# Kernel optimization log

Measured on AMD Instinct MI355X. Metric: run time of the kernel, lower is better.

Reference implementation:

```python
import jax, jax.numpy as jnp
import numpy as np

PAD_TOKEN_ID = 0
PAGE_SIZE = 64
BOUNDARY_IDS = (13, 30)


def setup_inputs() -> dict:
    B, L, V = 64, 16384, 32000
    P = L // PAGE_SIZE
    key = jax.random.key(0)
    k1, k2, k3 = jax.random.split(key, 3)
    input_ids = jax.random.randint(k1, (B, L), 0, V, dtype=jnp.int32)
    attention_mask = jnp.ones((B, L), dtype=jnp.int32)
    # token -> page index, exactly pos // page_size as SegmentPager would build
    token2page = jnp.broadcast_to(jnp.arange(L, dtype=jnp.int32) // PAGE_SIZE, (B, L))
    keep_pages = jax.random.bernoulli(k2, 0.3, (B, P))  # bool [B, P]
    query_pos = jax.random.randint(k3, (B,), 0, L, dtype=jnp.int32)
    return {
        'input_ids': input_ids,
        'attention_mask': attention_mask,
        'token2page': token2page,
        'keep_pages': keep_pages,
        'query_pos': query_pos,
    }


def reference(input_ids, attention_mask, token2page, keep_pages, query_pos):
    B, L = input_ids.shape
    valid = attention_mask.astype(bool)                         # token_valid [B,L]
    pos = jnp.arange(L, dtype=jnp.int32)

    # --- page-level keep mask gathered per token ---
    t2p = jnp.clip(token2page, 0, None)
    page_keep = jnp.take_along_axis(keep_pages, t2p, axis=1)    # [B,L] bool
    mask = valid & page_keep                                    # keep_token

    # --- force-keep the query tail: mask[qp:] |= valid[qp:] ---
    qp = jnp.clip(query_pos.astype(jnp.int32), 0, L - 1)        # [B]
    tail = pos[None, :] >= qp[:, None]
    mask = mask | (tail & valid)

    # --- sentence rescue in context [0, qp): if any token of a sentence is kept,
    #     keep all valid tokens of that sentence. Sentences are delimited by
    #     boundary tokens (segment = exclusive cumsum of boundary indicators). ---
    boundary = jnp.zeros_like(valid)
    for tid in BOUNDARY_IDS:
        boundary = boundary | (input_ids == tid)
    boundary = boundary & valid
    bcnt = boundary.astype(jnp.int32)
    seg = jnp.cumsum(bcnt, axis=1) - bcnt                       # sentence id per token
    in_ctx = pos[None, :] < qp[:, None]
    seg_d = jnp.where(in_ctx, seg, L)                           # dummy segment L for non-ctx
    flat_seg = (jnp.arange(B, dtype=jnp.int32)[:, None] * (L + 1) + seg_d).reshape(-1)
    keep_any = jax.ops.segment_max(mask.astype(jnp.int32).reshape(-1), flat_seg,
                                   num_segments=B * (L + 1))
    tok_keep = (keep_any[flat_seg] > 0).reshape(B, L)
    mask = mask | (in_ctx & valid & tok_keep)

    # --- fallback: if nothing kept, keep last valid token (or position 0) ---
    any_kept = mask.any(axis=1)
    any_valid = valid.any(axis=1)
    last_valid = jnp.where(any_valid, L - 1 - jnp.argmax(valid[:, ::-1], axis=1), 0)
    fallback = pos[None, :] == last_valid[:, None]
    mask = jnp.where(any_kept[:, None], mask, fallback)

    # --- stream compaction + left-justified padding (padded to L for static shape) ---
    order = jnp.argsort(jnp.logical_not(mask), axis=1)          # stable: kept indices first, in order
    lk = mask.sum(axis=1).astype(jnp.int32)                     # kept length per row
    attn = pos[None, :] < lk[:, None]
    ids_sorted = jnp.take_along_axis(input_ids, order, axis=1)
    ids_comp = jnp.where(attn, ids_sorted, PAD_TOKEN_ID)
    attn_comp = attn.astype(jnp.int32)
    pos_comp = jnp.where(attn, pos[None, :], 0)
    return ids_comp, attn_comp, pos_comp
```

## Files before the change

kernel.cpp:

```cpp
#include <hip/hip_runtime.h>
#include <stdint.h>

#define BB 64
#define LL 16384
#define PP 256
#define NT 1024
#define TT 16

__device__ __forceinline__ int block_exscan(int v, int tid, int* s_wave, int* s_total) {
    __syncthreads();
    const int lane = tid & 63;
    const int wv = tid >> 6;
    int inc = v;
#pragma unroll
    for (int off = 1; off < 64; off <<= 1) {
        int n = __shfl_up(inc, off, 64);
        if (lane >= off) inc += n;
    }
    if (lane == 63) s_wave[wv] = inc;
    __syncthreads();
    if (wv == 0) {
        int wval = (lane < 16) ? s_wave[lane] : 0;
        int winc = wval;
#pragma unroll
        for (int off = 1; off < 16; off <<= 1) {
            int n = __shfl_up(winc, off, 64);
            if (lane >= off) winc += n;
        }
        if (lane < 16) s_wave[lane] = winc - wval;
        if (lane == 15) *s_total = winc;
    }
    __syncthreads();
    return inc - v + s_wave[wv];
}

__global__ void __launch_bounds__(NT) seg_kernel(
    const int* __restrict__ g_ids,
    const int* __restrict__ g_amask,
    const int* __restrict__ g_t2p,
    const int* __restrict__ g_kp,
    const int* __restrict__ g_qp,
    int* __restrict__ g_out)
{
    __shared__ unsigned int segbits[LL / 32];
    __shared__ unsigned char kp[PP];
    __shared__ int s_wave[16];
    __shared__ int s_total;

    const int b = blockIdx.x;
    const int tid = threadIdx.x;
    const int tbase = tid * TT;
    const int rowoff = b * LL;

    for (int i = tid; i < LL / 32; i += NT) segbits[i] = 0u;
    if (tid < PP) kp[tid] = (g_kp[b * PP + tid] != 0);

    int qp = g_qp[b];
    qp = qp < 0 ? 0 : (qp > LL - 1 ? LL - 1 : qp);
    __syncthreads();

    int myids[TT];
    unsigned validbits = 0u, bndbits = 0u, mask1bits = 0u;
    {
        const int4* idp = (const int4*)(g_ids   + rowoff + tbase);
        const int4* amp = (const int4*)(g_amask + rowoff + tbase);
        const int4* tpp = (const int4*)(g_t2p   + rowoff + tbase);
#pragma unroll
        for (int jv = 0; jv < TT / 4; ++jv) {
            int4 iv = idp[jv];
            int4 av = amp[jv];
            int4 pv = tpp[jv];
            int idsv[4] = {iv.x, iv.y, iv.z, iv.w};
            int amv[4]  = {av.x, av.y, av.z, av.w};
            int tpv[4]  = {pv.x, pv.y, pv.z, pv.w};
#pragma unroll
            for (int k = 0; k < 4; ++k) {
                const int j = jv * 4 + k;
                myids[j] = idsv[k];
                const int va = (amv[k] != 0);
                const int bd = va && (idsv[k] == 13 || idsv[k] == 30);
                int pg = tpv[k];
                pg = pg < 0 ? 0 : (pg > PP - 1 ? PP - 1 : pg);
                const int pk = (kp[pg] != 0);
                const int gpos = tbase + j;
                const int m1 = va && (pk || gpos >= qp);
                validbits |= (unsigned)va << j;
                bndbits   |= (unsigned)bd << j;
                mask1bits |= (unsigned)m1 << j;
            }
        }
    }

    const int bcnt = __popc(bndbits);
    const int seg_base = block_exscan(bcnt, tid, s_wave, &s_total);

    unsigned ctxbits;
    {
        const int rel = qp - tbase;
        ctxbits = (rel <= 0) ? 0u : ((rel >= TT) ? 0xFFFFu : ((1u << rel) - 1u));
    }

    {
        unsigned cands = mask1bits & ctxbits;
        unsigned lsk = 0u;
        while (cands) {
            const int j = __ffs(cands) - 1;
            cands &= cands - 1;
            lsk |= 1u << __popc(bndbits & ((1u << j) - 1u));
        }
        while (lsk) {
            const int j2 = __ffs(lsk) - 1;
            lsk &= lsk - 1;
            const int s = seg_base + j2;
            const unsigned w = (unsigned)s >> 5, m = 1u << (s & 31);
            if ((segbits[w] & m) == 0u) atomicOr(&segbits[w], m);
        }
    }
    __syncthreads();

    unsigned mask2bits = mask1bits;
    {
        unsigned cand = validbits & ctxbits & ~mask1bits;
        while (cand) {
            const int j = __ffs(cand) - 1;
            cand &= cand - 1;
            const int s = seg_base + __popc(bndbits & ((1u << j) - 1u));
            if (segbits[(unsigned)s >> 5] & (1u << (s & 31))) mask2bits |= 1u << j;
        }
    }

    const int kc = __popc(mask2bits);
    const int cbase = block_exscan(kc, tid, s_wave, &s_total);
    int lk = s_total;

    if (lk == 0) {
        int lv = -1;
#pragma unroll
        for (int j = 0; j < TT; ++j)
            if ((validbits >> j) & 1u) lv = tbase + j;
#pragma unroll
        for (int off = 32; off >= 1; off >>= 1) {
            int n = __shfl_down(lv, off, 64);
            lv = lv > n ? lv : n;
        }
        __syncthreads();
        if ((tid & 63) == 0) s_wave[tid >> 6] = lv;
        __syncthreads();
        if (tid == 0) {
            int m = -1;
            for (int w = 0; w < 16; ++w) m = m > s_wave[w] ? m : s_wave[w];
            const int p = m < 0 ? 0 : m;
            g_out[rowoff + 0] = g_ids[rowoff + p];
        }
        lk = 1;
        mask2bits = 0u;
    }

    {
        int c = rowoff + cbase;
        unsigned mm = mask2bits;
        while (mm) {
            const int j = __ffs(mm) - 1;
            mm &= mm - 1;
            g_out[c++] = myids[j];
        }
    }

    {
        int* attn_out = g_out + (size_t)BB * LL;
        int* pos_out  = g_out + (size_t)2 * BB * LL;
#pragma unroll
        for (int jv = 0; jv < TT / 4; ++jv) {
            const int i0 = tbase + jv * 4;
            int4 a, p;
            a.x = (i0 + 0) < lk; a.y = (i0 + 1) < lk;
            a.z = (i0 + 2) < lk; a.w = (i0 + 3) < lk;
            p.x = (i0 + 0) < lk ? (i0 + 0) : 0;
            p.y = (i0 + 1) < lk ? (i0 + 1) : 0;
            p.z = (i0 + 2) < lk ? (i0 + 2) : 0;
            p.w = (i0 + 3) < lk ? (i0 + 3) : 0;
            *((int4*)(attn_out + rowoff + i0)) = a;
            *((int4*)(pos_out  + rowoff + i0)) = p;
        }
#pragma unroll
        for (int j = 0; j < TT; ++j) {
            const int i = tbase + j;
            if (i >= lk) g_out[rowoff + i] = 0;
        }
    }
}

extern "C" void kernel_launch(void* const* d_in, const int* in_sizes, int n_in,
                              void* d_out, int out_size, void* d_ws, size_t ws_size,
                              hipStream_t stream) {
    const int* ids  = (const int*)d_in[0];
    const int* am   = (const int*)d_in[1];
    const int* t2p  = (const int*)d_in[2];
    const int* kpg  = (const int*)d_in[3];
    const int* qp   = (const int*)d_in[4];
    int* out        = (int*)d_out;
    seg_kernel<<<BB, NT, 0, stream>>>(ids, am, t2p, kpg, qp, out);
}
```

Before: 93.48 us.

## Split row kernel into three kernels for mask build, scan, and compaction

Replaces the single kernel, which ran one 1024-thread block per row (64 blocks total), with three kernels. The first builds packed valid, boundary and keep bitmasks over a 8x64 grid. The second does a per-row word-level scan and sentence rescue on the compact bitmasks. The third compacts token ids and writes the outputs over 512 blocks. The aim is to fill the GPU's compute units for the bandwidth-heavy phases instead of leaving most idle. The cost is two extra launches, a workspace round trip, and re-reading input_ids.

```diff
diff --git a/kernel.cpp b/kernel.cpp
--- a/kernel.cpp
+++ b/kernel.cpp
@@ -4,13 +4,64 @@
 #define BB 64
 #define LL 16384
 #define PP 256
-#define NT 1024
-#define TT 16
-
-__device__ __forceinline__ int block_exscan(int v, int tid, int* s_wave, int* s_total) {
-    __syncthreads();
-    const int lane = tid & 63;
-    const int wv = tid >> 6;
+#define WW (LL / 32)
+#define NT2 512
+
+__global__ void __launch_bounds__(256) k1_masks(
+    const int* __restrict__ g_ids, const int* __restrict__ g_amask,
+    const int* __restrict__ g_t2p, const int* __restrict__ g_kp,
+    const int* __restrict__ g_qp,
+    unsigned* __restrict__ validw, unsigned* __restrict__ bndw,
+    unsigned* __restrict__ mask1w)
+{
+    __shared__ unsigned char kp[PP];
+    const int chunk = blockIdx.x;
+    const int row   = blockIdx.y;
+    const int t     = threadIdx.x;
+    if (t < PP) kp[t] = (g_kp[row * PP + t] != 0);
+    int qp = g_qp[row];
+    qp = qp < 0 ? 0 : (qp > LL - 1 ? LL - 1 : qp);
+    __syncthreads();
+
+    const int pos0 = chunk * 2048 + t * 8;
+    const int g = row * LL + pos0;
+    const int4* idp = (const int4*)(g_ids + g);
+    const int4* amp = (const int4*)(g_amask + g);
+    const int4* tpp = (const int4*)(g_t2p + g);
+    unsigned v8 = 0, b8 = 0, m8 = 0;
+#pragma unroll
+    for (int jv = 0; jv < 2; ++jv) {
+        int4 iv = idp[jv], av = amp[jv], pv = tpp[jv];
+        int idsv[4] = {iv.x, iv.y, iv.z, iv.w};
+        int amv[4]  = {av.x, av.y, av.z, av.w};
+        int tpv[4]  = {pv.x, pv.y, pv.z, pv.w};
+#pragma unroll
+        for (int k = 0; k < 4; ++k) {
+            const int j = jv * 4 + k;
+            const int va = (amv[k] != 0);
+            const int bd = va && (idsv[k] == 13 || idsv[k] == 30);
+            int pg = tpv[k];
+            pg = pg < 0 ? 0 : (pg > PP - 1 ? PP - 1 : pg);
+            const int m1 = va && (kp[pg] || (pos0 + j) >= qp);
+            v8 |= (unsigned)va << j;
+            b8 |= (unsigned)bd << j;
+            m8 |= (unsigned)m1 << j;
+        }
+    }
+    const int sub = t & 3, sh = 8 * sub;
+    unsigned vw = v8 << sh, bw = b8 << sh, mw = m8 << sh;
+    vw |= __shfl_xor(vw, 1, 64); vw |= __shfl_xor(vw, 2, 64);
+    bw |= __shfl_xor(bw, 1, 64); bw |= __shfl_xor(bw, 2, 64);
+    mw |= __shfl_xor(mw, 1, 64); mw |= __shfl_xor(mw, 2, 64);
+    if (sub == 0) {
+        const int widx = row * WW + chunk * 64 + (t >> 2);
+        validw[widx] = vw; bndw[widx] = bw; mask1w[widx] = mw;
+    }
+}
+
+__device__ __forceinline__ int exscan512(int v, int tid, int* s_wave, int* s_total) {
+    __syncthreads();
+    const int lane = tid & 63, wv = tid >> 6;
     int inc = v;
 #pragma unroll
     for (int off = 1; off < 64; off <<= 1) {
@@ -20,184 +71,182 @@
     if (lane == 63) s_wave[wv] = inc;
     __syncthreads();
     if (wv == 0) {
-        int wval = (lane < 16) ? s_wave[lane] : 0;
+        int wval = (lane < 8) ? s_wave[lane] : 0;
         int winc = wval;
 #pragma unroll
-        for (int off = 1; off < 16; off <<= 1) {
+        for (int off = 1; off < 8; off <<= 1) {
             int n = __shfl_up(winc, off, 64);
             if (lane >= off) winc += n;
         }
-        if (lane < 16) s_wave[lane] = winc - wval;
-        if (lane == 15) *s_total = winc;
+        if (lane < 8) s_wave[lane] = winc - wval;
+        if (lane == 7) *s_total = winc;
     }
     __syncthreads();
     return inc - v + s_wave[wv];
 }
 
-__global__ void __launch_bounds__(NT) seg_kernel(
-    const int* __restrict__ g_ids,
-    const int* __restrict__ g_amask,
-    const int* __restrict__ g_t2p,
-    const int* __restrict__ g_kp,
-    const int* __restrict__ g_qp,
+__global__ void __launch_bounds__(NT2) k2_scan(
+    const unsigned* __restrict__ validw, const unsigned* __restrict__ bndw,
+    const unsigned* __restrict__ mask1w, const int* __restrict__ g_qp,
+    unsigned* __restrict__ mask2w, int* __restrict__ wordscan,
+    int* __restrict__ lkarr)
+{
+    __shared__ unsigned segbits[WW];
+    __shared__ int s_wave[8];
+    __shared__ int s_total;
+    __shared__ int s_fb;
+    const int row = blockIdx.x;
+    const int t = threadIdx.x;
+    segbits[t] = 0u;
+    int qp = g_qp[row];
+    qp = qp < 0 ? 0 : (qp > LL - 1 ? LL - 1 : qp);
+    const unsigned vwd = validw[row * WW + t];
+    const unsigned bwd = bndw[row * WW + t];
+    const unsigned mwd = mask1w[row * WW + t];
+
+    const int segbase = exscan512(__popc(bwd), t, s_wave, &s_total);
+
+    const int rel = qp - t * 32;
+    const unsigned ctx = rel <= 0 ? 0u : (rel >= 32 ? 0xFFFFFFFFu : ((1u << rel) - 1u));
+
+    {
+        unsigned cands = mwd & ctx;
+        if (bwd == 0u) {
+            if (cands) {
+                const unsigned w_ = (unsigned)segbase >> 5, m_ = 1u << (segbase & 31);
+                if ((segbits[w_] & m_) == 0u) atomicOr(&segbits[w_], m_);
+            }
+        } else {
+            while (cands) {
+                const int j = __ffs(cands) - 1;
+                cands &= cands - 1;
+                const int s = segbase + __popc(bwd & ((1u << j) - 1u));
+                const unsigned w_ = (unsigned)s >> 5, m_ = 1u << (s & 31);
+                if ((segbits[w_] & m_) == 0u) atomicOr(&segbits[w_], m_);
+            }
+        }
+    }
+    __syncthreads();
+
+    unsigned m2 = mwd;
+    {
+        unsigned cand = vwd & ctx & ~mwd;
+        if (bwd == 0u) {
+            if (cand && ((segbits[(unsigned)segbase >> 5] >> (segbase & 31)) & 1u)) m2 |= cand;
+        } else {
+            while (cand) {
+                const int j = __ffs(cand) - 1;
+                cand &= cand - 1;
+                const int s = segbase + __popc(bwd & ((1u << j) - 1u));
+                if ((segbits[(unsigned)s >> 5] >> (s & 31)) & 1u) m2 |= 1u << j;
+            }
+        }
+    }
+
+    int cb = exscan512(__popc(m2), t, s_wave, &s_total);
+    int lk = s_total;
+
+    if (lk == 0) {
+        int lastv = vwd ? t * 32 + (31 - __clz(vwd)) : -1;
+#pragma unroll
+        for (int off = 32; off >= 1; off >>= 1) {
+            int n = __shfl_down(lastv, off, 64);
+            lastv = lastv > n ? lastv : n;
+        }
+        __syncthreads();
+        if ((t & 63) == 0) s_wave[t >> 6] = lastv;
+        __syncthreads();
+        if (t == 0) {
+            int m = -1;
+            for (int w = 0; w < 8; ++w) m = m > s_wave[w] ? m : s_wave[w];
+            s_fb = m < 0 ? 0 : m;
+        }
+        __syncthreads();
+        const int fb = s_fb, fw = fb >> 5;
+        m2 = (t == fw) ? (1u << (fb & 31)) : 0u;
+        cb = (t > fw) ? 1 : 0;
+        lk = 1;
+    }
+
+    mask2w[row * WW + t] = m2;
+    wordscan[row * WW + t] = cb;
+    if (t == 0) lkarr[row] = lk;
+}
+
+__global__ void __launch_bounds__(256) k3_write(
+    const int* __restrict__ g_ids, const unsigned* __restrict__ mask2w,
+    const int* __restrict__ wordscan, const int* __restrict__ lkarr,
     int* __restrict__ g_out)
 {
-    __shared__ unsigned int segbits[LL / 32];
-    __shared__ unsigned char kp[PP];
-    __shared__ int s_wave[16];
-    __shared__ int s_total;
-
-    const int b = blockIdx.x;
-    const int tid = threadIdx.x;
-    const int tbase = tid * TT;
-    const int rowoff = b * LL;
-
-    for (int i = tid; i < LL / 32; i += NT) segbits[i] = 0u;
-    if (tid < PP) kp[tid] = (g_kp[b * PP + tid] != 0);
-
-    int qp = g_qp[b];
-    qp = qp < 0 ? 0 : (qp > LL - 1 ? LL - 1 : qp);
-    __syncthreads();
-
-    int myids[TT];
-    unsigned validbits = 0u, bndbits = 0u, mask1bits = 0u;
-    {
-        const int4* idp = (const int4*)(g_ids   + rowoff + tbase);
-        const int4* amp = (const int4*)(g_amask + rowoff + tbase);
-        const int4* tpp = (const int4*)(g_t2p   + rowoff + tbase);
-#pragma unroll
-        for (int jv = 0; jv < TT / 4; ++jv) {
-            int4 iv = idp[jv];
-            int4 av = amp[jv];
-            int4 pv = tpp[jv];
-            int idsv[4] = {iv.x, iv.y, iv.z, iv.w};
-            int amv[4]  = {av.x, av.y, av.z, av.w};
-            int tpv[4]  = {pv.x, pv.y, pv.z, pv.w};
-#pragma unroll
-            for (int k = 0; k < 4; ++k) {
-                const int j = jv * 4 + k;
-                myids[j] = idsv[k];
-                const int va = (amv[k] != 0);
-                const int bd = va && (idsv[k] == 13 || idsv[k] == 30);
-                int pg = tpv[k];
-                pg = pg < 0 ? 0 : (pg > PP - 1 ? PP - 1 : pg);
-                const int pk = (kp[pg] != 0);
-                const int gpos = tbase + j;
-                const int m1 = va && (pk || gpos >= qp);
-                validbits |= (unsigned)va << j;
-                bndbits   |= (unsigned)bd << j;
-                mask1bits |= (unsigned)m1 << j;
-            }
-        }
-    }
-
-    const int bcnt = __popc(bndbits);
-    const int seg_base = block_exscan(bcnt, tid, s_wave, &s_total);
-
-    unsigned ctxbits;
-    {
-        const int rel = qp - tbase;
-        ctxbits = (rel <= 0) ? 0u : ((rel >= TT) ? 0xFFFFu : ((1u << rel) - 1u));
-    }
-
-    {
-        unsigned cands = mask1bits & ctxbits;
-        unsigned lsk = 0u;
-        while (cands) {
-            const int j = __ffs(cands) - 1;
-            cands &= cands - 1;
-            lsk |= 1u << __popc(bndbits & ((1u << j) - 1u));
-        }
-        while (lsk) {
-            const int j2 = __ffs(lsk) - 1;
-            lsk &= lsk - 1;
-            const int s = seg_base + j2;
-            const unsigned w = (unsigned)s >> 5, m = 1u << (s & 31);
-            if ((segbits[w] & m) == 0u) atomicOr(&segbits[w], m);
-        }
-    }
-    __syncthreads();
-
-    unsigned mask2bits = mask1bits;
-    {
-        unsigned cand = validbits & ctxbits & ~mask1bits;
-        while (cand) {
-            const int j = __ffs(cand) - 1;
-            cand &= cand - 1;
-            const int s = seg_base + __popc(bndbits & ((1u << j) - 1u));
-            if (segbits[(unsigned)s >> 5] & (1u << (s & 31))) mask2bits |= 1u << j;
-        }
-    }
-
-    const int kc = __popc(mask2bits);
-    const int cbase = block_exscan(kc, tid, s_wave, &s_total);
-    int lk = s_total;
-
-    if (lk == 0) {
-        int lv = -1;
-#pragma unroll
-        for (int j = 0; j < TT; ++j)
-            if ((validbits >> j) & 1u) lv = tbase + j;
-#pragma unroll
-        for (int off = 32; off >= 1; off >>= 1) {
-            int n = __shfl_down(lv, off, 64);
-            lv = lv > n ? lv : n;
-        }
-        __syncthreads();
-        if ((tid & 63) == 0) s_wave[tid >> 6] = lv;
-        __syncthreads();
-        if (tid == 0) {
-            int m = -1;
-            for (int w = 0; w < 16; ++w) m = m > s_wave[w] ? m : s_wave[w];
-            const int p = m < 0 ? 0 : m;
-            g_out[rowoff + 0] = g_ids[rowoff + p];
-        }
-        lk = 1;
-        mask2bits = 0u;
-    }
-
-    {
-        int c = rowoff + cbase;
-        unsigned mm = mask2bits;
+    const int chunk = blockIdx.x;
+    const int row   = blockIdx.y;
+    const int t     = threadIdx.x;
+    const int pos0 = chunk * 2048 + t * 8;
+    const int widx = row * WW + (pos0 >> 5);
+    const unsigned m2 = mask2w[widx];
+    const int base = wordscan[widx];
+    const int lk = lkarr[row];
+    const int sub = t & 3;
+    const unsigned mybits = (m2 >> (8 * sub)) & 0xffu;
+    const int off = base + __popc(m2 & ((1u << (8 * sub)) - 1u));
+
+    const int g = row * LL + pos0;
+    const int4* idp = (const int4*)(g_ids + g);
+    int4 i0 = idp[0], i1 = idp[1];
+
+    const int c = row * LL + off;
+    if (mybits == 0xffu && (off & 3) == 0) {
+        ((int4*)(g_out + c))[0] = i0;
+        ((int4*)(g_out + c))[1] = i1;
+    } else if (mybits) {
+        int idsv[8] = {i0.x, i0.y, i0.z, i0.w, i1.x, i1.y, i1.z, i1.w};
+        int cc = c;
+        unsigned mm = mybits;
         while (mm) {
             const int j = __ffs(mm) - 1;
             mm &= mm - 1;
-            g_out[c++] = myids[j];
-        }
-    }
-
-    {
-        int* attn_out = g_out + (size_t)BB * LL;
-        int* pos_out  = g_out + (size_t)2 * BB * LL;
-#pragma unroll
-        for (int jv = 0; jv < TT / 4; ++jv) {
-            const int i0 = tbase + jv * 4;
-            int4 a, p;
-            a.x = (i0 + 0) < lk; a.y = (i0 + 1) < lk;
-            a.z = (i0 + 2) < lk; a.w = (i0 + 3) < lk;
-            p.x = (i0 + 0) < lk ? (i0 + 0) : 0;
-            p.y = (i0 + 1) < lk ? (i0 + 1) : 0;
-            p.z = (i0 + 2) < lk ? (i0 + 2) : 0;
-            p.w = (i0 + 3) < lk ? (i0 + 3) : 0;
-            *((int4*)(attn_out + rowoff + i0)) = a;
-            *((int4*)(pos_out  + rowoff + i0)) = p;
-        }
-#pragma unroll
-        for (int j = 0; j < TT; ++j) {
-            const int i = tbase + j;
-            if (i >= lk) g_out[rowoff + i] = 0;
-        }
-    }
+            g_out[cc++] = idsv[j];
+        }
+    }
+
+    if (pos0 + 7 >= lk) {
+#pragma unroll
+        for (int j = 0; j < 8; ++j)
+            if (pos0 + j >= lk) g_out[g + j] = 0;
+    }
+
+    int* attn = g_out + (size_t)BB * LL;
+    int* pos  = g_out + (size_t)2 * BB * LL;
+    int4 a0, a1, p0, p1;
+    a0.x = (pos0 + 0) < lk; a0.y = (pos0 + 1) < lk; a0.z = (pos0 + 2) < lk; a0.w = (pos0 + 3) < lk;
+    a1.x = (pos0 + 4) < lk; a1.y = (pos0 + 5) < lk; a1.z = (pos0 + 6) < lk; a1.w = (pos0 + 7) < lk;
+    p0.x = a0.x ? pos0 + 0 : 0; p0.y = a0.y ? pos0 + 1 : 0; p0.z = a0.z ? pos0 + 2 : 0; p0.w = a0.w ? pos0 + 3 : 0;
+    p1.x = a1.x ? pos0 + 4 : 0; p1.y = a1.y ? pos0 + 5 : 0; p1.z = a1.z ? pos0 + 6 : 0; p1.w = a1.w ? pos0 + 7 : 0;
+    ((int4*)(attn + g))[0] = a0;
+    ((int4*)(attn + g))[1] = a1;
+    ((int4*)(pos + g))[0] = p0;
+    ((int4*)(pos + g))[1] = p1;
 }
 
 extern "C" void kernel_launch(void* const* d_in, const int* in_sizes, int n_in,
                               void* d_out, int out_size, void* d_ws, size_t ws_size,
                               hipStream_t stream) {
-    const int* ids  = (const int*)d_in[0];
-    const int* am   = (const int*)d_in[1];
-    const int* t2p  = (const int*)d_in[2];
-    const int* kpg  = (const int*)d_in[3];
-    const int* qp   = (const int*)d_in[4];
-    int* out        = (int*)d_out;
-    seg_kernel<<<BB, NT, 0, stream>>>(ids, am, t2p, kpg, qp, out);
-}
+    const int* ids = (const int*)d_in[0];
+    const int* am  = (const int*)d_in[1];
+    const int* t2p = (const int*)d_in[2];
+    const int* kpg = (const int*)d_in[3];
+    const int* qp  = (const int*)d_in[4];
+    int* out       = (int*)d_out;
+
+    unsigned* validw = (unsigned*)d_ws;
+    unsigned* bndw   = validw + BB * WW;
+    unsigned* mask1w = bndw + BB * WW;
+    unsigned* mask2w = mask1w + BB * WW;
+    int* wordscan    = (int*)(mask2w + BB * WW);
+    int* lkarr       = wordscan + BB * WW;
+
+    dim3 gridA(8, BB);
+    k1_masks<<<gridA, 256, 0, stream>>>(ids, am, t2p, kpg, qp, validw, bndw, mask1w);
+    k2_scan<<<BB, NT2, 0, stream>>>(validw, bndw, mask1w, qp, mask2w, wordscan, lkarr);
+    k3_write<<<gridA, 256, 0, stream>>>(ids, mask2w, wordscan, lkarr, out);
+}
```

Result: faster. 83.76 us (median of 2 runs) (-10.4%).
